# Kernel tuning notes

Measured on AMD Instinct MI355X. Metric: run time of the kernel, lower is better.

Reference implementation:

```python
import jax, jax.numpy as jnp
import numpy as np

Q, M, D = 4096, 100000, 1536

def _l2norm(x, eps=1e-12):
    return x / jnp.maximum(jnp.linalg.norm(x, axis=1, keepdims=True), eps)

def setup_inputs() -> dict:
    key = jax.random.key(0)
    kq, km = jax.random.split(key)
    # patch features are L2-normalized in _extract_patches (F.normalize p=2)
    query = _l2norm(jax.random.normal(kq, (Q, D), dtype=jnp.float32))
    memory = _l2norm(jax.random.normal(km, (M, D), dtype=jnp.float32))
    return {"query": query, "memory": memory}

def reference(query, memory):
    # torch.cdist(query, memory) (p=2) followed by min over memory dim.
    # dist^2 = |q|^2 + |m|^2 - 2 q.m  -> sqrt, clamped at 0 for numerics.
    q2 = jnp.sum(query * query, axis=1, keepdims=True)          # [Q, 1]
    m2 = jnp.sum(memory * memory, axis=1)                        # [M]
    d2 = q2 + m2[None, :] - 2.0 * (query @ memory.T)             # [Q, M]
    dists = jnp.sqrt(jnp.maximum(d2, 0.0))
    nn_dists = jnp.min(dists, axis=1)                            # [Q]
    anomaly_score = jnp.max(nn_dists)                            # scalar, predict()'s score
    return nn_dists, anomaly_score
```

## Files before the change

### kernel.cpp

```cpp
#include <hip/hip_runtime.h>
#include <hip/hip_bf16.h>
#include <float.h>


#define QN 4096
#define MN 100000
#define MP 100096
#define DN 1536
#define BK 32
#define NKIT (DN / BK)

typedef __attribute__((ext_vector_type(8))) short short8;
typedef __attribute__((ext_vector_type(4))) float float4v;
typedef __attribute__((ext_vector_type(4))) short short4v;
typedef __attribute__((address_space(1))) const unsigned g_u32;
typedef __attribute__((address_space(3))) unsigned l_u32;

__device__ __forceinline__ short f2bf(float f) {
    unsigned u = __float_as_uint(f);
    u += 0x7FFFu + ((u >> 16) & 1u);
    return (short)(u >> 16);
}
__device__ __forceinline__ unsigned encf(float f) {
    unsigned u = __float_as_uint(f);
    return (u & 0x80000000u) ? ~u : (u | 0x80000000u);
}
__device__ __forceinline__ float decf(unsigned e) {
    unsigned u = (e & 0x80000000u) ? (e & 0x7FFFFFFFu) : ~e;
    return __uint_as_float(u);
}
__device__ __forceinline__ void gload_lds16(const void* g, void* l) {
    __builtin_amdgcn_global_load_lds((g_u32*)g, (l_u32*)l, 16, 0, 0);
}

__global__ void init_min(unsigned* __restrict__ dminEnc) {
    int i = blockIdx.x * blockDim.x + threadIdx.x;
    if (i < QN) dminEnc[i] = 0xFF7FFFFFu;
}

__global__ void cvt_bf16(const float* __restrict__ src, short* __restrict__ dst,
                         long n_valid, long n_total) {
    long i = ((long)blockIdx.x * blockDim.x + threadIdx.x) * 4;
    if (i >= n_total) return;
    if (i + 4 <= n_valid) {
        float4 v = *(const float4*)(src + i);
        short4v o = { f2bf(v.x), f2bf(v.y), f2bf(v.z), f2bf(v.w) };
        *(short4v*)(dst + i) = o;
    } else {
        for (int j = 0; j < 4; ++j)
            if (i + j < n_total) dst[i + j] = (i + j < n_valid) ? f2bf(src[i + j]) : 0;
    }
}

__global__ __launch_bounds__(256)
void nn_gemm_bf16(const short* __restrict__ qB, const short* __restrict__ mB,
                  unsigned* __restrict__ dminEnc)
{
    __shared__ __align__(16) short As[128 * BK];
    __shared__ __align__(16) short Bs[128 * BK];
    __shared__ unsigned qmin[128];

    const int tid  = threadIdx.x;
    const int lane = tid & 63;
    const int wave = tid >> 6;
    const int wrow = wave >> 1;
    const int wcol = wave & 1;
    const int quad = lane >> 4;
    const int l16  = lane & 15;

    const int qb = blockIdx.x * 128;
    const int mb = blockIdx.y * 128;

    if (tid < 128) qmin[tid] = 0xFFFFFFFFu;

    const int srow = wave * 32 + (lane >> 2);
    const int scol = (lane & 3) * 8;
    const short* gA0 = qB + (size_t)(qb + srow) * DN + scol;
    const short* gA1 = gA0 + (size_t)16 * DN;
    const short* gB0 = mB + (size_t)(mb + srow) * DN + scol;
    const short* gB1 = gB0 + (size_t)16 * DN;
    short* lA0 = As + (wave * 32) * BK;
    short* lA1 = As + (wave * 32 + 16) * BK;
    short* lB0 = Bs + (wave * 32) * BK;
    short* lB1 = Bs + (wave * 32 + 16) * BK;

    float4v acc[4][4];
#pragma unroll
    for (int mi = 0; mi < 4; ++mi)
#pragma unroll
        for (int ni = 0; ni < 4; ++ni)
            acc[mi][ni] = (float4v){0.f, 0.f, 0.f, 0.f};

    for (int kk = 0; kk < NKIT; ++kk) {
        const size_t ko = (size_t)kk * BK;
        gload_lds16(gA0 + ko, lA0);
        gload_lds16(gA1 + ko, lA1);
        gload_lds16(gB0 + ko, lB0);
        gload_lds16(gB1 + ko, lB1);
        __syncthreads();

        short8 af[4], bf[4];
#pragma unroll
        for (int mi = 0; mi < 4; ++mi)
            af[mi] = *(const short8*)&As[(wrow * 64 + mi * 16 + l16) * BK + quad * 8];
#pragma unroll
        for (int ni = 0; ni < 4; ++ni)
            bf[ni] = *(const short8*)&Bs[(wcol * 64 + ni * 16 + l16) * BK + quad * 8];

#pragma unroll
        for (int mi = 0; mi < 4; ++mi)
#pragma unroll
            for (int ni = 0; ni < 4; ++ni)
                acc[mi][ni] = __builtin_amdgcn_mfma_f32_16x16x32_bf16(
                    af[mi], bf[ni], acc[mi][ni], 0, 0, 0);
        __syncthreads();
    }

#pragma unroll
    for (int mi = 0; mi < 4; ++mi) {
#pragma unroll
        for (int r = 0; r < 4; ++r) {
            float v = FLT_MAX;
#pragma unroll
            for (int ni = 0; ni < 4; ++ni) {
                int gcol = mb + wcol * 64 + ni * 16 + l16;
                float d2 = fmaf(-2.0f, acc[mi][ni][r], 2.0f);
                v = fminf(v, (gcol < MN) ? d2 : FLT_MAX);
            }
            v = fminf(v, __shfl_xor(v, 1));
            v = fminf(v, __shfl_xor(v, 2));
            v = fminf(v, __shfl_xor(v, 4));
            v = fminf(v, __shfl_xor(v, 8));
            if (l16 == 0) {
                int rloc = wrow * 64 + mi * 16 + quad * 4 + r;
                atomicMin(&qmin[rloc], encf(v));
            }
        }
    }
    __syncthreads();
    if (tid < 128) atomicMin(&dminEnc[qb + tid], qmin[tid]);
}

#define LDSS 40
__global__ __launch_bounds__(256, 2)
void nn_gemm_f32(const float* __restrict__ query, const float* __restrict__ memory,
                 unsigned* __restrict__ dminEnc)
{
    __shared__ __align__(16) short As[128 * LDSS];
    __shared__ __align__(16) short Bs[128 * LDSS];
    __shared__ unsigned qmin[128];

    const int tid = threadIdx.x, lane = tid & 63, wave = tid >> 6;
    const int wrow = wave >> 1, wcol = wave & 1, quad = lane >> 4, l16 = lane & 15;
    const int qb = blockIdx.x * 128, mb = blockIdx.y * 128;
    if (tid < 128) qmin[tid] = 0xFFFFFFFFu;

    int rowS[4], c4S[4];
    const float *aPtr[4], *bPtr[4];
    bool bValid[4];
#pragma unroll
    for (int s = 0; s < 4; ++s) {
        int idx = s * 256 + tid, row = idx >> 3, c4 = idx & 7;
        rowS[s] = row; c4S[s] = c4;
        aPtr[s] = query + (size_t)(qb + row) * DN + c4 * 4;
        int gr = mb + row;
        bValid[s] = (gr < MN);
        bPtr[s] = memory + (size_t)(bValid[s] ? gr : 0) * DN + c4 * 4;
    }
    float4 aReg[4], bReg[4];
#pragma unroll
    for (int s = 0; s < 4; ++s) {
        aReg[s] = *(const float4*)(aPtr[s]);
        bReg[s] = bValid[s] ? *(const float4*)(bPtr[s]) : make_float4(0.f, 0.f, 0.f, 0.f);
    }
    float4v acc[4][4];
#pragma unroll
    for (int mi = 0; mi < 4; ++mi)
#pragma unroll
        for (int ni = 0; ni < 4; ++ni) acc[mi][ni] = (float4v){0.f, 0.f, 0.f, 0.f};

    for (int kk = 0; kk < NKIT; ++kk) {
#pragma unroll
        for (int s = 0; s < 4; ++s) {
            short4v pa = { f2bf(aReg[s].x), f2bf(aReg[s].y), f2bf(aReg[s].z), f2bf(aReg[s].w) };
            short4v pb = { f2bf(bReg[s].x), f2bf(bReg[s].y), f2bf(bReg[s].z), f2bf(bReg[s].w) };
            *(short4v*)&As[rowS[s] * LDSS + c4S[s] * 4] = pa;
            *(short4v*)&Bs[rowS[s] * LDSS + c4S[s] * 4] = pb;
        }
        __syncthreads();
        if (kk + 1 < NKIT) {
            const int ko = (kk + 1) * BK;
#pragma unroll
            for (int s = 0; s < 4; ++s) {
                aReg[s] = *(const float4*)(aPtr[s] + ko);
                bReg[s] = bValid[s] ? *(const float4*)(bPtr[s] + ko)
                                    : make_float4(0.f, 0.f, 0.f, 0.f);
            }
        }
        short8 af[4], bf[4];
#pragma unroll
        for (int mi = 0; mi < 4; ++mi)
            af[mi] = *(const short8*)&As[(wrow * 64 + mi * 16 + l16) * LDSS + quad * 8];
#pragma unroll
        for (int ni = 0; ni < 4; ++ni)
            bf[ni] = *(const short8*)&Bs[(wcol * 64 + ni * 16 + l16) * LDSS + quad * 8];
#pragma unroll
        for (int mi = 0; mi < 4; ++mi)
#pragma unroll
            for (int ni = 0; ni < 4; ++ni)
                acc[mi][ni] = __builtin_amdgcn_mfma_f32_16x16x32_bf16(
                    af[mi], bf[ni], acc[mi][ni], 0, 0, 0);
        __syncthreads();
    }
#pragma unroll
    for (int mi = 0; mi < 4; ++mi) {
#pragma unroll
        for (int r = 0; r < 4; ++r) {
            float v = FLT_MAX;
#pragma unroll
            for (int ni = 0; ni < 4; ++ni) {
                int gcol = mb + wcol * 64 + ni * 16 + l16;
                float d2 = fmaf(-2.0f, acc[mi][ni][r], 2.0f);
                v = fminf(v, (gcol < MN) ? d2 : FLT_MAX);
            }
            v = fminf(v, __shfl_xor(v, 1));
            v = fminf(v, __shfl_xor(v, 2));
            v = fminf(v, __shfl_xor(v, 4));
            v = fminf(v, __shfl_xor(v, 8));
            if (l16 == 0)
                atomicMin(&qmin[wrow * 64 + mi * 16 + quad * 4 + r], encf(v));
        }
    }
    __syncthreads();
    if (tid < 128) atomicMin(&dminEnc[qb + tid], qmin[tid]);
}

__global__ void finalize(const unsigned* __restrict__ dminEnc, float* __restrict__ out) {
    __shared__ float red[256];
    const int tid = threadIdx.x;
    float mx = 0.f;
    for (int i = tid; i < QN; i += 256) {
        float d2 = decf(dminEnc[i]);
        float d = sqrtf(fmaxf(d2, 0.f));
        out[i] = d;
        mx = fmaxf(mx, d);
    }
    red[tid] = mx;
    __syncthreads();
    for (int s = 128; s > 0; s >>= 1) {
        if (tid < s) red[tid] = fmaxf(red[tid], red[tid + s]);
        __syncthreads();
    }
    if (tid == 0) out[QN] = red[0];
}

extern "C" void kernel_launch(void* const* d_in, const int* in_sizes, int n_in,
                              void* d_out, int out_size, void* d_ws, size_t ws_size,
                              hipStream_t stream)
{
    const float* query  = (const float*)d_in[0];
    const float* memory = (const float*)d_in[1];
    float* out = (float*)d_out;

    const size_t memB_elems = (size_t)MP * DN;
    const size_t qB_elems   = (size_t)QN * DN;
    const size_t need = memB_elems * 2 + qB_elems * 2 + (size_t)QN * 4;

    if (ws_size >= need) {
        short* mB = (short*)d_ws;
        short* qB = mB + memB_elems;
        unsigned* dminEnc = (unsigned*)(qB + qB_elems);

        hipLaunchKernelGGL(init_min, dim3((QN + 255) / 256), dim3(256), 0, stream, dminEnc);
        {
            long nv = (long)MN * DN, nt = (long)memB_elems;
            int blocks = (int)((nt / 4 + 255) / 256);
            hipLaunchKernelGGL(cvt_bf16, dim3(blocks), dim3(256), 0, stream,
                               memory, mB, nv, nt);
        }
        {
            long nv = (long)qB_elems, nt = (long)qB_elems;
            int blocks = (int)((nt / 4 + 255) / 256);
            hipLaunchKernelGGL(cvt_bf16, dim3(blocks), dim3(256), 0, stream,
                               query, qB, nv, nt);
        }
        hipLaunchKernelGGL(nn_gemm_bf16, dim3(QN / 128, MP / 128), dim3(256), 0, stream,
                           qB, mB, dminEnc);
        hipLaunchKernelGGL(finalize, dim3(1), dim3(256), 0, stream, dminEnc, out);
    } else {
        unsigned* dminEnc = (unsigned*)d_ws;
        hipLaunchKernelGGL(init_min, dim3((QN + 255) / 256), dim3(256), 0, stream, dminEnc);
        hipLaunchKernelGGL(nn_gemm_f32, dim3(QN / 128, (MN + 127) / 128), dim3(256), 0, stream,
                           query, memory, dminEnc);
        hipLaunchKernelGGL(finalize, dim3(1), dim3(256), 0, stream, dminEnc, out);
    }
}
```

Baseline: 2.267 ms.

## Replace 128x128 bf16 NN GEMM with double-buffered 256x256 eight-wave pipelined kernel

The bf16 nearest-neighbour kernel is rewritten to use 256x256 output tiles with 512 threads (8 waves, 2x4 layout). Each wave now accumulates 128x64. K-steps are 64 wide, and the LDS buffers are double-buffered and swizzled. Direct global-to-LDS loads are interleaved with MFMA phases using explicit s_barrier, vmcnt waits, sched_barrier and setprio. The aim is to raise arithmetic intensity and hide global-load latency, which the old kernel exposed because it synchronised twice per 32-wide K-step with no prefetch. In exchange, register and LDS pressure rise, occupancy likely falls to one block per CU, and the hand-scheduled waitcnt logic is fragile.

```diff
diff --git a/kernel.cpp b/kernel.cpp
--- a/kernel.cpp
+++ b/kernel.cpp
@@ -7,6 +7,7 @@
 #define MN 100000
 #define MP 100096
 #define DN 1536
+#define NT 24
 #define BK 32
 #define NKIT (DN / BK)
 
@@ -52,93 +53,183 @@
     }
 }
 
-__global__ __launch_bounds__(256)
-void nn_gemm_bf16(const short* __restrict__ qB, const short* __restrict__ mB,
-                  unsigned* __restrict__ dminEnc)
+#define SUB_OFF(b, h, R, C) ((((((b) * 2 + (h)) * 8 + (R)) * 2) + (C)) * 512)
+
+__global__ __launch_bounds__(512, 2)
+void nn_gemm_bf16_256(const short* __restrict__ qB, const short* __restrict__ mB,
+                      unsigned* __restrict__ dminEnc)
 {
-    __shared__ __align__(16) short As[128 * BK];
-    __shared__ __align__(16) short Bs[128 * BK];
-    __shared__ unsigned qmin[128];
-
-    const int tid  = threadIdx.x;
-    const int lane = tid & 63;
-    const int wave = tid >> 6;
-    const int wrow = wave >> 1;
-    const int wcol = wave & 1;
-    const int quad = lane >> 4;
-    const int l16  = lane & 15;
-
-    const int qb = blockIdx.x * 128;
-    const int mb = blockIdx.y * 128;
-
-    if (tid < 128) qmin[tid] = 0xFFFFFFFFu;
-
-    const int srow = wave * 32 + (lane >> 2);
-    const int scol = (lane & 3) * 8;
-    const short* gA0 = qB + (size_t)(qb + srow) * DN + scol;
-    const short* gA1 = gA0 + (size_t)16 * DN;
-    const short* gB0 = mB + (size_t)(mb + srow) * DN + scol;
-    const short* gB1 = gB0 + (size_t)16 * DN;
-    short* lA0 = As + (wave * 32) * BK;
-    short* lA1 = As + (wave * 32 + 16) * BK;
-    short* lB0 = Bs + (wave * 32) * BK;
-    short* lB1 = Bs + (wave * 32 + 16) * BK;
-
-    float4v acc[4][4];
-#pragma unroll
-    for (int mi = 0; mi < 4; ++mi)
-#pragma unroll
-        for (int ni = 0; ni < 4; ++ni)
-            acc[mi][ni] = (float4v){0.f, 0.f, 0.f, 0.f};
-
-    for (int kk = 0; kk < NKIT; ++kk) {
-        const size_t ko = (size_t)kk * BK;
-        gload_lds16(gA0 + ko, lA0);
-        gload_lds16(gA1 + ko, lA1);
-        gload_lds16(gB0 + ko, lB0);
-        gload_lds16(gB1 + ko, lB1);
-        __syncthreads();
-
-        short8 af[4], bf[4];
-#pragma unroll
-        for (int mi = 0; mi < 4; ++mi)
-            af[mi] = *(const short8*)&As[(wrow * 64 + mi * 16 + l16) * BK + quad * 8];
-#pragma unroll
-        for (int ni = 0; ni < 4; ++ni)
-            bf[ni] = *(const short8*)&Bs[(wcol * 64 + ni * 16 + l16) * BK + quad * 8];
-
-#pragma unroll
-        for (int mi = 0; mi < 4; ++mi)
-#pragma unroll
-            for (int ni = 0; ni < 4; ++ni)
-                acc[mi][ni] = __builtin_amdgcn_mfma_f32_16x16x32_bf16(
-                    af[mi], bf[ni], acc[mi][ni], 0, 0, 0);
-        __syncthreads();
-    }
-
-#pragma unroll
-    for (int mi = 0; mi < 4; ++mi) {
+    __shared__ short A_lds[2 * 2 * 8 * 2 * 512];
+    __shared__ short B_lds[2 * 2 * 8 * 2 * 512];
+
+    const int tid = threadIdx.x;
+    const int l   = tid & 63;
+    const int w   = tid >> 6;
+    const int wm  = w >> 2;
+    const int wn  = w & 3;
+    const int l15 = l & 15;
+    const int q4  = l >> 4;
+
+    const int qb = blockIdx.x * 256;
+    const int mb = blockIdx.y * 256;
+
+    const int rlane = l >> 2;
+    const int csw   = ((l & 3) ^ ((l >> 5) << 1)) * 8;
+    const int sh    = w >> 2;
+    const int saR   = w & 3;
+    const int sbR   = ((w >> 1) & 1) * 4 + (w & 1);
+
+    const short* pAlo = qB + (size_t)(qb + sh * 128 + saR * 16 + rlane) * DN + csw;
+    const short* pAhi = pAlo + (size_t)64 * DN;
+    const short* pBc0 = mB + (size_t)(mb + sh * 128 + sbR * 16 + rlane) * DN + csw;
+    const short* pBc1 = pBc0 + (size_t)32 * DN;
+
+    const int inoff = l15 * 64 + ((q4 ^ (((l >> 3) & 1) << 1))) * 16;
+    const char* aP = (const char*)A_lds + wm * 16384 + inoff;
+    const char* bP = (const char*)B_lds + (wn >> 1) * 16384 + (wn & 1) * 8192 + inoff;
+
+    short8 af[4][2], bf[2][2];
+    float4v acc[8][4];
+#pragma unroll
+    for (int fi = 0; fi < 8; ++fi)
+#pragma unroll
+        for (int cj = 0; cj < 4; ++cj)
+            acc[fi][cj] = (float4v){0.f, 0.f, 0.f, 0.f};
+
+#define STAGE_ALO(b, ko) do { \
+        gload_lds16(pAlo + (ko),      &A_lds[SUB_OFF(b, sh, saR,     0)]); \
+        gload_lds16(pAlo + (ko) + 32, &A_lds[SUB_OFF(b, sh, saR,     1)]); } while (0)
+#define STAGE_AHI(b, ko) do { \
+        gload_lds16(pAhi + (ko),      &A_lds[SUB_OFF(b, sh, saR + 4, 0)]); \
+        gload_lds16(pAhi + (ko) + 32, &A_lds[SUB_OFF(b, sh, saR + 4, 1)]); } while (0)
+#define STAGE_BC0(b, ko) do { \
+        gload_lds16(pBc0 + (ko),      &B_lds[SUB_OFF(b, sh, sbR,     0)]); \
+        gload_lds16(pBc0 + (ko) + 32, &B_lds[SUB_OFF(b, sh, sbR,     1)]); } while (0)
+#define STAGE_BC1(b, ko) do { \
+        gload_lds16(pBc1 + (ko),      &B_lds[SUB_OFF(b, sh, sbR + 2, 0)]); \
+        gload_lds16(pBc1 + (ko) + 32, &B_lds[SUB_OFF(b, sh, sbR + 2, 1)]); } while (0)
+
+#define LDA(b, RH) do { _Pragma("unroll") \
+        for (int m_ = 0; m_ < 4; ++m_) { \
+            af[m_][0] = *(const short8*)(aP + (b) * 32768 + ((RH) * 4 + m_) * 2048); \
+            af[m_][1] = *(const short8*)(aP + (b) * 32768 + ((RH) * 4 + m_) * 2048 + 1024); } } while (0)
+#define LDB(b, CH) do { _Pragma("unroll") \
+        for (int n_ = 0; n_ < 2; ++n_) { \
+            bf[n_][0] = *(const short8*)(bP + (b) * 32768 + ((CH) * 2 + n_) * 2048); \
+            bf[n_][1] = *(const short8*)(bP + (b) * 32768 + ((CH) * 2 + n_) * 2048 + 1024); } } while (0)
+
+#define MMA(RH, CH) do { _Pragma("unroll") \
+        for (int m_ = 0; m_ < 4; ++m_) { _Pragma("unroll") \
+            for (int n_ = 0; n_ < 2; ++n_) { \
+                acc[(RH) * 4 + m_][(CH) * 2 + n_] = __builtin_amdgcn_mfma_f32_16x16x32_bf16( \
+                    af[m_][0], bf[n_][0], acc[(RH) * 4 + m_][(CH) * 2 + n_], 0, 0, 0); \
+                acc[(RH) * 4 + m_][(CH) * 2 + n_] = __builtin_amdgcn_mfma_f32_16x16x32_bf16( \
+                    af[m_][1], bf[n_][1], acc[(RH) * 4 + m_][(CH) * 2 + n_], 0, 0, 0); } } } while (0)
+
+#define MID(RH, CH) \
+        __builtin_amdgcn_sched_barrier(0); \
+        __builtin_amdgcn_s_barrier(); \
+        asm volatile("s_waitcnt lgkmcnt(0)" ::: "memory"); \
+        __builtin_amdgcn_sched_barrier(0); \
+        __builtin_amdgcn_s_setprio(1); \
+        MMA(RH, CH); \
+        __builtin_amdgcn_s_setprio(0); \
+        __builtin_amdgcn_sched_barrier(0);
+#define TAIL \
+        __builtin_amdgcn_s_barrier(); \
+        __builtin_amdgcn_sched_barrier(0);
+#define TAIL_VM6 \
+        asm volatile("s_waitcnt vmcnt(6)" ::: "memory"); \
+        __builtin_amdgcn_s_barrier(); \
+        __builtin_amdgcn_sched_barrier(0);
+#define TAIL_VM0 \
+        asm volatile("s_waitcnt vmcnt(0)" ::: "memory"); \
+        __builtin_amdgcn_s_barrier(); \
+        __builtin_amdgcn_sched_barrier(0);
+
+    STAGE_ALO(0, 0); STAGE_AHI(0, 0); STAGE_BC0(0, 0); STAGE_BC1(0, 0);
+    STAGE_ALO(1, 64); STAGE_BC1(1, 64); STAGE_AHI(1, 64);
+    __builtin_amdgcn_sched_barrier(0);
+    asm volatile("s_waitcnt vmcnt(6) lgkmcnt(0)" ::: "memory");
+    __builtin_amdgcn_s_barrier();
+    __builtin_amdgcn_sched_barrier(0);
+
+    for (int it = 0; it < NT / 2 - 1; ++it) {
+        const int kT1 = (it * 2 + 1) * 64;
+        const int kT2 = kT1 + 64;
+        const int kT3 = kT1 + 128;
+        LDA(0, 0); LDB(0, 0); STAGE_BC0(1, kT1);
+        MID(0, 0) TAIL
+        LDB(0, 1); STAGE_ALO(0, kT2);
+        MID(0, 1) TAIL
+        LDA(0, 1); STAGE_BC1(0, kT2);
+        MID(1, 1) TAIL
+        LDB(0, 0); STAGE_AHI(0, kT2);
+        MID(1, 0) TAIL_VM6
+        LDA(1, 0); LDB(1, 0); STAGE_BC0(0, kT2);
+        MID(0, 0) TAIL
+        LDB(1, 1); STAGE_ALO(1, kT3);
+        MID(0, 1) TAIL
+        LDA(1, 1); STAGE_BC1(1, kT3);
+        MID(1, 1) TAIL
+        LDB(1, 0); STAGE_AHI(1, kT3);
+        MID(1, 0) TAIL_VM6
+    }
+    LDA(0, 0); LDB(0, 0); STAGE_BC0(1, (NT - 1) * 64);
+    MID(0, 0) TAIL
+    LDB(0, 1);
+    MID(0, 1) TAIL
+    LDA(0, 1);
+    MID(1, 1) TAIL
+    LDB(0, 0);
+    MID(1, 0) TAIL_VM0
+    LDA(1, 0); LDB(1, 0);
+    MID(0, 0) TAIL
+    LDB(1, 1);
+    MID(0, 1) TAIL
+    LDA(1, 1);
+    MID(1, 1) TAIL
+    LDB(1, 0);
+    MID(1, 0)
+
+#undef STAGE_ALO
+#undef STAGE_AHI
+#undef STAGE_BC0
+#undef STAGE_BC1
+#undef LDA
+#undef LDB
+#undef MMA
+#undef MID
+#undef TAIL
+#undef TAIL_VM6
+#undef TAIL_VM0
+
+    unsigned* qmin = (unsigned*)A_lds;
+    __syncthreads();
+    if (tid < 256) qmin[tid] = 0xFFFFFFFFu;
+    __syncthreads();
+
+#pragma unroll
+    for (int fi = 0; fi < 8; ++fi) {
 #pragma unroll
         for (int r = 0; r < 4; ++r) {
             float v = FLT_MAX;
 #pragma unroll
-            for (int ni = 0; ni < 4; ++ni) {
-                int gcol = mb + wcol * 64 + ni * 16 + l16;
-                float d2 = fmaf(-2.0f, acc[mi][ni][r], 2.0f);
+            for (int cj = 0; cj < 4; ++cj) {
+                const int gcol = mb + wn * 64 + cj * 16 + l15;
+                const float d2 = fmaf(-2.0f, acc[fi][cj][r], 2.0f);
                 v = fminf(v, (gcol < MN) ? d2 : FLT_MAX);
             }
             v = fminf(v, __shfl_xor(v, 1));
             v = fminf(v, __shfl_xor(v, 2));
             v = fminf(v, __shfl_xor(v, 4));
             v = fminf(v, __shfl_xor(v, 8));
-            if (l16 == 0) {
-                int rloc = wrow * 64 + mi * 16 + quad * 4 + r;
-                atomicMin(&qmin[rloc], encf(v));
-            }
-        }
-    }
-    __syncthreads();
-    if (tid < 128) atomicMin(&dminEnc[qb + tid], qmin[tid]);
+            if (l15 == 0)
+                atomicMin(&qmin[wm * 128 + fi * 16 + q4 * 4 + r], encf(v));
+        }
+    }
+    __syncthreads();
+    if (tid < 256) atomicMin(&dminEnc[qb + tid], qmin[tid]);
 }
 
 #define LDSS 40
@@ -197,19 +288,19 @@
                                     : make_float4(0.f, 0.f, 0.f, 0.f);
             }
         }
-        short8 af[4], bf[4];
+        short8 af[4], bfr[4];
 #pragma unroll
         for (int mi = 0; mi < 4; ++mi)
             af[mi] = *(const short8*)&As[(wrow * 64 + mi * 16 + l16) * LDSS + quad * 8];
 #pragma unroll
         for (int ni = 0; ni < 4; ++ni)
-            bf[ni] = *(const short8*)&Bs[(wcol * 64 + ni * 16 + l16) * LDSS + quad * 8];
+            bfr[ni] = *(const short8*)&Bs[(wcol * 64 + ni * 16 + l16) * LDSS + quad * 8];
 #pragma unroll
         for (int mi = 0; mi < 4; ++mi)
 #pragma unroll
             for (int ni = 0; ni < 4; ++ni)
                 acc[mi][ni] = __builtin_amdgcn_mfma_f32_16x16x32_bf16(
-                    af[mi], bf[ni], acc[mi][ni], 0, 0, 0);
+                    af[mi], bfr[ni], acc[mi][ni], 0, 0, 0);
         __syncthreads();
     }
 #pragma unroll
@@ -284,7 +375,7 @@
             hipLaunchKernelGGL(cvt_bf16, dim3(blocks), dim3(256), 0, stream,
                                query, qB, nv, nt);
         }
-        hipLaunchKernelGGL(nn_gemm_bf16, dim3(QN / 128, MP / 128), dim3(256), 0, stream,
+        hipLaunchKernelGGL(nn_gemm_bf16_256, dim3(QN / 256, MP / 256), dim3(512), 0, stream,
                            qB, mB, dminEnc);
         hipLaunchKernelGGL(finalize, dim3(1), dim3(256), 0, stream, dminEnc, out);
     } else {
```

Result: no change. 2.302 ms (+1.6%).
